# Kernel tuning notes

Measured on AMD Instinct MI355X. Metric: run time of the kernel, lower is better.

Reference implementation:

```python
import jax, jax.numpy as jnp
from jax import lax
import numpy as np

EPS = 1e-5

def _conv(x, w, b, s, p):
    # torch Conv2d: weight [O,I,kH,kW], NCHW
    y = lax.conv_general_dilated(x, w, (s, s), [(p, p), (p, p)],
                                 dimension_numbers=('NCHW', 'OIHW', 'NCHW'))
    return y + b[None, :, None, None]

def _convT(x, w, b, s, p):
    # torch ConvTranspose2d: weight [I,O,kH,kW]; equivalent to lhs-dilated conv
    wf = jnp.flip(w, (2, 3)).transpose(1, 0, 2, 3)  # -> [O,I,kH,kW]
    q = w.shape[2] - 1 - p
    y = lax.conv_general_dilated(x, wf, (1, 1), [(q, q), (q, q)],
                                 lhs_dilation=(s, s),
                                 dimension_numbers=('NCHW', 'OIHW', 'NCHW'))
    return y + b[None, :, None, None]

def _bn(x, g, b, m, v):
    # eval-mode BatchNorm2d with running stats
    s = g / jnp.sqrt(v + EPS)
    return x * s[None, :, None, None] + (b - m * s)[None, :, None, None]

def _forward(x, ew1, eb1, bn1g, bn1b, bn1m, bn1v, ew2, eb2, bn2g, bn2b, bn2m, bn2v,
             ew3, eb3, bn3g, bn3b, bn3m, bn3v, ew4, eb4, bn4g, bn4b, bn4m, bn4v,
             fc21w, fc21b, fc22w, fc22b, fc3w, fc3b,
             cw1, cb1, cbn1g, cbn1b, cbn1m, cbn1v, cw2, cb2, emb,
             dw1, db1, dbn1g, dbn1b, dbn1m, dbn1v, dw2, db2, dbn2g, dbn2b, dbn2m, dbn2v,
             dw3, db3, dbn3g, dbn3b, dbn3m, dbn3v, dw4, db4, dbn4g, dbn4b, dbn4m, dbn4v,
             ow, ob):
    relu = jax.nn.relu
    N = x.shape[0]
    # ---- encoder ----
    h = relu(_bn(_conv(x, ew1, eb1, 2, 1), bn1g, bn1b, bn1m, bn1v))   # [N,16,32,32]
    h = relu(_bn(_conv(h, ew2, eb2, 2, 1), bn2g, bn2b, bn2m, bn2v))   # [N,16,16,16]
    h = relu(_bn(_conv(h, ew3, eb3, 2, 1), bn3g, bn3b, bn3m, bn3v))   # [N,16,9,9]
    h = relu(_bn(_conv(h, ew4, eb4, 1, 0), bn4g, bn4b, bn4m, bn4v))   # [N,128,9,9]
    hl = h.reshape(N, -1)                                              # [N,10368]
    mu = hl @ fc21w + fc21b
    logvar = hl @ fc22w + fc22b
    z = mu  # eval-mode reparameterize returns mu
    # ---- vq_decode ----
    co = relu(z @ fc3w + fc3b)                                         # [N,10368]
    col = co.reshape(N, 128, 9, 9)
    ze = relu(_bn(_convT(col, cw1, cb1, 1, 0), cbn1g, cbn1b, cbn1m, cbn1v))
    z_e_x = _convT(ze, cw2, cb2, 1, 0)                                 # [N,32,9,9]
    zt = z_e_x.transpose(0, 2, 3, 1)                                   # [N,H,W,C]
    # ||z - e||^2 expanded (avoids [N,H,W,C,K] intermediate)
    d = ((zt * zt).sum(-1, keepdims=True)
         - 2.0 * jnp.einsum('nhwc,kc->nhwk', zt, emb)
         + (emb * emb).sum(-1))                                        # [N,H,W,K]
    latents = jnp.argmin(d, axis=-1)                                   # [N,H,W] int
    z_q = emb[latents]                                                 # [N,H,W,C]
    z_q_x = z_q.transpose(0, 3, 1, 2)                                  # [N,32,9,9]
    # ---- decoder ----
    g = relu(_bn(_convT(z_q_x, dw1, db1, 1, 0), dbn1g, dbn1b, dbn1m, dbn1v))  # [N,16,9,9]
    g = relu(_bn(_convT(g, dw2, db2, 2, 1), dbn2g, dbn2b, dbn2m, dbn2v))      # [N,16,18,18]
    g = relu(_bn(_convT(g, dw3, db3, 2, 1), dbn3g, dbn3b, dbn3m, dbn3v))      # [N,16,34,34]
    g = relu(_bn(_convT(g, dw4, db4, 2, 0), dbn4g, dbn4b, dbn4m, dbn4v))      # [N,16,68,68]
    x_tilde = _convT(g, ow, ob, 1, 0)                                         # [N,1,68,68]
    return (x_tilde, z, mu, logvar, z_e_x, z_q_x, latents)


def setup_inputs() -> dict:
    key = jax.random.key(0)
    ks = iter(jax.random.split(key, 64))
    def rn(shape, scale=0.05):
        return scale * jax.random.normal(next(ks), shape, jnp.float32)
    inp = {'x': jax.random.normal(next(ks), (512, 1, 64, 64), jnp.float32)}
    wspecs = {
        'ew1': (16, 1, 4, 4), 'eb1': (16,), 'ew2': (16, 16, 4, 4), 'eb2': (16,),
        'ew3': (16, 16, 2, 2), 'eb3': (16,), 'ew4': (128, 16, 1, 1), 'eb4': (128,),
        'fc21w': (10368, 64), 'fc21b': (64,), 'fc22w': (10368, 64), 'fc22b': (64,),
        'fc3w': (64, 10368), 'fc3b': (10368,),
        'cw1': (128, 32, 1, 1), 'cb1': (32,), 'cw2': (32, 32, 1, 1), 'cb2': (32,),
        'dw1': (32, 16, 1, 1), 'db1': (16,), 'dw2': (16, 16, 4, 4), 'db2': (16,),
        'dw3': (16, 16, 2, 2), 'db3': (16,), 'dw4': (16, 16, 2, 2), 'db4': (16,),
        'ow': (16, 1, 1, 1),
    }
    for n, s in wspecs.items():
        inp[n] = rn(s)
    inp['ob'] = jnp.full((1,), 0.5, jnp.float32)
    for ch, pre in [(16, 'bn1'), (16, 'bn2'), (16, 'bn3'), (128, 'bn4'), (32, 'cbn1'),
                    (16, 'dbn1'), (16, 'dbn2'), (16, 'dbn3'), (16, 'dbn4')]:
        inp[pre + 'g'] = jnp.ones((ch,), jnp.float32)
        inp[pre + 'b'] = jnp.zeros((ch,), jnp.float32)
        inp[pre + 'm'] = jnp.zeros((ch,), jnp.float32)
        inp[pre + 'v'] = jnp.ones((ch,), jnp.float32)
    inp['emb'] = rn((512, 32), 1.0 / 512)
    return inp


def reference(x, ew1, eb1, bn1g, bn1b, bn1m, bn1v, ew2, eb2, bn2g, bn2b, bn2m, bn2v,
              ew3, eb3, bn3g, bn3b, bn3m, bn3v, ew4, eb4, bn4g, bn4b, bn4m, bn4v,
              fc21w, fc21b, fc22w, fc22b, fc3w, fc3b,
              cw1, cb1, cbn1g, cbn1b, cbn1m, cbn1v, cw2, cb2, emb,
              dw1, db1, dbn1g, dbn1b, dbn1m, dbn1v, dw2, db2, dbn2g, dbn2b, dbn2m, dbn2v,
              dw3, db3, dbn3g, dbn3b, dbn3m, dbn3v, dw4, db4, dbn4g, dbn4b, dbn4m, dbn4v,
              ow, ob):
    return _forward(x, ew1, eb1, bn1g, bn1b, bn1m, bn1v, ew2, eb2, bn2g, bn2b, bn2m, bn2v,
                    ew3, eb3, bn3g, bn3b, bn3m, bn3v, ew4, eb4, bn4g, bn4b, bn4m, bn4v,
                    fc21w, fc21b, fc22w, fc22b, fc3w, fc3b,
                    cw1, cb1, cbn1g, cbn1b, cbn1m, cbn1v, cw2, cb2, emb,
                    dw1, db1, dbn1g, dbn1b, dbn1m, dbn1v, dw2, db2, dbn2g, dbn2b, dbn2m, dbn2v,
                    dw3, db3, dbn3g, dbn3b, dbn3m, dbn3v, dw4, db4, dbn4g, dbn4b, dbn4m, dbn4v,
                    ow, ob)
```

## Files before the change

kernel.cpp:

```cpp
#include <hip/hip_runtime.h>
#include <math.h>
#include <float.h>

#define BN_EPS 1e-5f

__device__ __forceinline__ float bn_apply(float y, float g, float b, float m, float v) {
  float s = g / sqrtf(v + BN_EPS);
  return y * s + (b - m * s);
}

__global__ void k_conv1(const float* __restrict__ x, const float* __restrict__ w,
                        const float* __restrict__ bias,
                        const float* __restrict__ g, const float* __restrict__ bb,
                        const float* __restrict__ bm, const float* __restrict__ bv,
                        float* __restrict__ out) {
  int t = blockIdx.x * 256 + threadIdx.x;
  int xo = t & 31, yo = (t >> 5) & 31, n = t >> 10;
  int iy0 = 2 * yo - 1, ix0 = 2 * xo - 1;
  const float* xb = x + n * 4096;
  float p[16];
#pragma unroll
  for (int ky = 0; ky < 4; ++ky)
#pragma unroll
    for (int kx = 0; kx < 4; ++kx) {
      int iy = iy0 + ky, ix = ix0 + kx;
      bool ok = (iy >= 0) & (iy < 64) & (ix >= 0) & (ix < 64);
      p[ky * 4 + kx] = ok ? xb[iy * 64 + ix] : 0.0f;
    }
  float* ob = out + n * 16384 + yo * 32 + xo;
#pragma unroll
  for (int o = 0; o < 16; ++o) {
    float acc = bias[o];
#pragma unroll
    for (int k = 0; k < 16; ++k) acc += p[k] * w[o * 16 + k];
    acc = bn_apply(acc, g[o], bb[o], bm[o], bv[o]);
    ob[o * 1024] = fmaxf(acc, 0.0f);
  }
}

__global__ void k_conv2(const float* __restrict__ A, const float* __restrict__ w,
                        const float* __restrict__ bias,
                        const float* __restrict__ g, const float* __restrict__ bb,
                        const float* __restrict__ bm, const float* __restrict__ bv,
                        float* __restrict__ out) {
  __shared__ float ws[4096];
  for (int i = threadIdx.x; i < 4096; i += 256) ws[i] = w[i];
  __syncthreads();
  int t = blockIdx.x * 256 + threadIdx.x;
  int x8 = t & 7, yo = (t >> 3) & 15, n = t >> 7;
  int iy0 = 2 * yo - 1;
  const float* Ab = A + n * 16384;
  float acc[2][16];
#pragma unroll
  for (int o = 0; o < 16; ++o) { float bvv = bias[o]; acc[0][o] = bvv; acc[1][o] = bvv; }
  for (int i = 0; i < 16; ++i) {
    float p[2][16];
#pragma unroll
    for (int px = 0; px < 2; ++px) {
      int ix0 = 2 * (x8 + px * 8) - 1;
#pragma unroll
      for (int ky = 0; ky < 4; ++ky)
#pragma unroll
        for (int kx = 0; kx < 4; ++kx) {
          int iy = iy0 + ky, ix = ix0 + kx;
          bool ok = (iy >= 0) & (iy < 32) & (ix >= 0) & (ix < 32);
          p[px][ky * 4 + kx] = ok ? Ab[i * 1024 + iy * 32 + ix] : 0.0f;
        }
    }
#pragma unroll
    for (int o = 0; o < 16; ++o) {
#pragma unroll
      for (int k = 0; k < 16; ++k) {
        float wv = ws[(o * 16 + i) * 16 + k];
        acc[0][o] += p[0][k] * wv;
        acc[1][o] += p[1][k] * wv;
      }
    }
  }
#pragma unroll
  for (int o = 0; o < 16; ++o) {
    float s = g[o] / sqrtf(bv[o] + BN_EPS);
    float sh = bb[o] - bm[o] * s;
    float* ob = out + (n * 16 + o) * 256 + yo * 16;
    ob[x8]     = fmaxf(acc[0][o] * s + sh, 0.0f);
    ob[x8 + 8] = fmaxf(acc[1][o] * s + sh, 0.0f);
  }
}

__global__ void __launch_bounds__(256) k_c34(const float* __restrict__ in,
    const float* __restrict__ w3, const float* __restrict__ b3,
    const float* __restrict__ g3, const float* __restrict__ bb3,
    const float* __restrict__ bm3, const float* __restrict__ bv3,
    const float* __restrict__ w4, const float* __restrict__ b4,
    const float* __restrict__ g4, const float* __restrict__ bb4,
    const float* __restrict__ bm4, const float* __restrict__ bv4,
    float* __restrict__ hl) {
  __shared__ float xin[4096];
  __shared__ float w3s[1024];
  __shared__ float c3s[16 * 81];
  __shared__ float k3a[16], k3b[16];
  __shared__ float k4a[128], k4b[128];
  int bx = blockIdx.x;
  int n = bx >> 1, half = bx & 1;
  int t = threadIdx.x;
  {
    const float4* iv = (const float4*)(in + n * 4096);
    float4* xv = (float4*)xin;
#pragma unroll
    for (int q = 0; q < 4; ++q) xv[t + 256 * q] = iv[t + 256 * q];
    if (t < 256) w3s[t] = w3[t];
    if (t >= 256 - 0) {}
    for (int i = t + 256; i < 1024; i += 256) w3s[i] = w3[i];
  }
  if (t < 16) {
    float s = g3[t] / sqrtf(bv3[t] + BN_EPS);
    k3a[t] = s;
    k3b[t] = b3[t] * s + (bb3[t] - bm3[t] * s);
  } else if (t >= 64 && t < 192) {
    int o = t - 64;
    float s = g4[o] / sqrtf(bv4[o] + BN_EPS);
    k4a[o] = s;
    k4b[o] = b4[o] * s + (bb4[o] - bm4[o] * s);
  }
  __syncthreads();
  for (int idx = t; idx < 1296; idx += 256) {
    int o = idx / 81, p = idx - o * 81;
    int yo = p / 9, xo = p - yo * 9;
    int iy0 = 2 * yo - 1, ix0 = 2 * xo - 1;
    bool ytop = iy0 >= 0, ybot = iy0 + 1 < 16;
    bool xlft = ix0 >= 0, xrgt = ix0 + 1 < 16;
    int iyt = ytop ? iy0 : 0, iyb = ybot ? iy0 + 1 : 15;
    int ixl = xlft ? ix0 : 0, ixr = xrgt ? ix0 + 1 : 15;
    float acc = 0.0f;
#pragma unroll
    for (int i = 0; i < 16; ++i) {
      const float* ch = xin + i * 256;
      float p0 = (ytop & xlft) ? ch[iyt * 16 + ixl] : 0.0f;
      float p1 = (ytop & xrgt) ? ch[iyt * 16 + ixr] : 0.0f;
      float p2 = (ybot & xlft) ? ch[iyb * 16 + ixl] : 0.0f;
      float p3 = (ybot & xrgt) ? ch[iyb * 16 + ixr] : 0.0f;
      float4 wv = *(const float4*)&w3s[(o * 16 + i) * 4];
      acc += p0 * wv.x + p1 * wv.y + p2 * wv.z + p3 * wv.w;
    }
    c3s[idx] = fmaxf(acc * k3a[o] + k3b[o], 0.0f);
  }
  __syncthreads();
  int lane = t & 63;
  int og = __builtin_amdgcn_readfirstlane(t >> 6);
  int o0 = half * 64 + og * 16;
  float* ob = hl + n * 10368;
#pragma unroll
  for (int pass = 0; pass < 2; ++pass) {
    int p = pass * 64 + lane;
    bool ok = p < 81; int pc = ok ? p : 80;
    float acc[16];
#pragma unroll
    for (int oo = 0; oo < 16; ++oo) acc[oo] = 0.0f;
#pragma unroll
    for (int i = 0; i < 16; ++i) {
      float v = c3s[i * 81 + pc];
#pragma unroll
      for (int oo = 0; oo < 16; ++oo)
        acc[oo] = fmaf(v, w4[(o0 + oo) * 16 + i], acc[oo]);
    }
    if (ok) {
#pragma unroll
      for (int oo = 0; oo < 16; ++oo) {
        int o = o0 + oo;
        ob[o * 81 + p] = fmaxf(acc[oo] * k4a[o] + k4b[o], 0.0f);
      }
    }
  }
}

__global__ void __launch_bounds__(256) k_gemm1(const float* __restrict__ hl,
                                               const float* __restrict__ w21,
                                               const float* __restrict__ w22,
                                               float* __restrict__ part) {
  __shared__ __align__(16) float hs[64 * 27];
  __shared__ __align__(16) float wsh[27 * 128];
  int kc = blockIdx.x, nt = blockIdx.y, t = threadIdx.x;
  int n0 = nt * 64, k0 = kc * 162;
  int jg = t & 31, ng = t >> 5;
  float acc[8][4];
#pragma unroll
  for (int i = 0; i < 8; ++i)
#pragma unroll
    for (int q = 0; q < 4; ++q) acc[i][q] = 0.0f;
  for (int s = 0; s < 6; ++s) {
    int ks = k0 + s * 27;
    __syncthreads();
    for (int idx = t; idx < 1728; idx += 256) {
      int r = idx / 27, c = idx - r * 27;
      hs[idx] = hl[(n0 + r) * 10368 + ks + c];
    }
    for (int idx = t; idx < 3456; idx += 256) {
      int r = idx >> 7, c = idx & 127;
      wsh[idx] = (c < 64) ? w21[(ks + r) * 64 + c] : w22[(ks + r) * 64 + (c - 64)];
    }
    __syncthreads();
#pragma unroll
    for (int kk = 0; kk < 27; ++kk) {
      float4 wv = *(const float4*)&wsh[kk * 128 + jg * 4];
#pragma unroll
      for (int i = 0; i < 8; ++i) {
        float h = hs[(ng * 8 + i) * 27 + kk];
        acc[i][0] = fmaf(h, wv.x, acc[i][0]);
        acc[i][1] = fmaf(h, wv.y, acc[i][1]);
        acc[i][2] = fmaf(h, wv.z, acc[i][2]);
        acc[i][3] = fmaf(h, wv.w, acc[i][3]);
      }
    }
  }
#pragma unroll
  for (int i = 0; i < 8; ++i) {
    int n = n0 + ng * 8 + i;
    float4 v = make_float4(acc[i][0], acc[i][1], acc[i][2], acc[i][3]);
    *(float4*)&part[(size_t)(kc * 512 + n) * 128 + jg * 4] = v;
  }
}

__global__ void k_fc_red(const float* __restrict__ part, const float* __restrict__ b21,
                         const float* __restrict__ b22, float* __restrict__ z,
                         float* __restrict__ mu, float* __restrict__ lv) {
  int t = blockIdx.x * 256 + threadIdx.x;
  int j = t & 127, n = t >> 7;
  float s = 0.0f;
  for (int kc = 0; kc < 64; ++kc) s += part[(size_t)(kc * 512 + n) * 128 + j];
  if (j < 64) { float r = s + b21[j]; z[n * 64 + j] = r; mu[n * 64 + j] = r; }
  else        { lv[n * 64 + (j - 64)] = s + b22[j - 64]; }
}

__global__ void k_fc3(const float* __restrict__ z, const float* __restrict__ w,
                      const float* __restrict__ b, float* __restrict__ E) {
  int m = blockIdx.x * 128 + threadIdx.x;
  int n0 = blockIdx.y * 32;
  float acc[32];
#pragma unroll
  for (int nn = 0; nn < 32; ++nn) acc[nn] = 0.0f;
  for (int j = 0; j < 64; ++j) {
    float wv = w[j * 10368 + m];
    const float* zb = z + n0 * 64 + j;
#pragma unroll
    for (int nn = 0; nn < 32; ++nn) acc[nn] += zb[nn * 64] * wv;
  }
  float bvv = b[m];
  float* Eb = E + n0 * 10368 + m;
#pragma unroll
  for (int nn = 0; nn < 32; ++nn) Eb[nn * 10368] = fmaxf(acc[nn] + bvv, 0.0f);
}

__global__ void __launch_bounds__(256) k_cw(const float* __restrict__ E,
                     const float* __restrict__ w1, const float* __restrict__ b1,
                     const float* __restrict__ g, const float* __restrict__ bb,
                     const float* __restrict__ bm, const float* __restrict__ bv,
                     const float* __restrict__ w2, const float* __restrict__ b2,
                     float* __restrict__ zex, float* __restrict__ zt) {
  __shared__ float ze_s[2592];
  int n = blockIdx.x, t = threadIdx.x;
  int lane = t & 63;
  int o0 = __builtin_amdgcn_readfirstlane(t >> 6) * 8;
  const float* co = E + n * 10368;
#pragma unroll
  for (int pass = 0; pass < 2; ++pass) {
    int p = pass * 64 + lane;
    bool ok = p < 81; int pc = ok ? p : 80;
    float acc[8];
#pragma unroll
    for (int oo = 0; oo < 8; ++oo) acc[oo] = b1[o0 + oo];
    for (int i = 0; i < 128; ++i) {
      float v = co[i * 81 + pc];
#pragma unroll
      for (int oo = 0; oo < 8; ++oo)
        acc[oo] = fmaf(v, w1[i * 32 + o0 + oo], acc[oo]);
    }
#pragma unroll
    for (int oo = 0; oo < 8; ++oo) {
      int o = o0 + oo;
      float r = bn_apply(acc[oo], g[o], bb[o], bm[o], bv[o]);
      if (ok) ze_s[o * 81 + p] = fmaxf(r, 0.0f);
    }
  }
  __syncthreads();
  float* zb = zex + n * 2592;
  float* ztb = zt + n * 81 * 32;
#pragma unroll
  for (int pass = 0; pass < 2; ++pass) {
    int p = pass * 64 + lane;
    bool ok = p < 81; int pc = ok ? p : 80;
    float acc[8];
#pragma unroll
    for (int oo = 0; oo < 8; ++oo) acc[oo] = b2[o0 + oo];
    for (int j = 0; j < 32; ++j) {
      float v = ze_s[j * 81 + pc];
#pragma unroll
      for (int oo = 0; oo < 8; ++oo)
        acc[oo] = fmaf(v, w2[j * 32 + o0 + oo], acc[oo]);
    }
    if (ok) {
#pragma unroll
      for (int oo = 0; oo < 8; ++oo) {
        zb[(o0 + oo) * 81 + p] = acc[oo];
        ztb[p * 32 + o0 + oo] = acc[oo];
      }
    }
  }
}

__global__ void k_ee(const float* __restrict__ emb, float* __restrict__ ee) {
  int k = blockIdx.x * 256 + threadIdx.x;
  if (k < 512) {
    const float4* e = (const float4*)(emb + k * 32);
    float s = 0.0f;
#pragma unroll
    for (int q = 0; q < 8; ++q) {
      float4 v = e[q];
      s += v.x * v.x + v.y * v.y + v.z * v.z + v.w * v.w;
    }
    ee[k] = s;
  }
}

__global__ void __launch_bounds__(256) k_vq2(const float* __restrict__ zt,
                                             const float* __restrict__ emb,
                                             const float* __restrict__ ee,
                                             float* __restrict__ lat_out,
                                             float* __restrict__ zqx) {
  __shared__ float bd_s[4][64];
  __shared__ int   bi_s[4][64];
  __shared__ int   bif[64];
  int t = threadIdx.x;
  int lane = t & 63, sub = t >> 6;
  int sub_u = __builtin_amdgcn_readfirstlane(sub);
  int pix = blockIdx.x * 64 + lane;
  float z[32];
  {
    const float4* zr = (const float4*)(zt + (size_t)pix * 32);
#pragma unroll
    for (int q = 0; q < 8; ++q) {
      float4 v = zr[q];
      z[q * 4] = v.x; z[q * 4 + 1] = v.y; z[q * 4 + 2] = v.z; z[q * 4 + 3] = v.w;
    }
  }
  const float* ebase = emb + sub_u * 128 * 32;
  const float* eeb   = ee + sub_u * 128;
  int kbase = sub_u * 128;
  float best = FLT_MAX;
  int bi = kbase;
  for (int kk = 0; kk < 128; kk += 2) {
    const float* e0 = ebase + kk * 32;
    const float* e1 = e0 + 32;
    float d0a = 0.f, d0b = 0.f, d1a = 0.f, d1b = 0.f;
#pragma unroll
    for (int c = 0; c < 32; c += 2) {
      d0a = fmaf(z[c], e0[c], d0a);
      d0b = fmaf(z[c + 1], e0[c + 1], d0b);
      d1a = fmaf(z[c], e1[c], d1a);
      d1b = fmaf(z[c + 1], e1[c + 1], d1b);
    }
    float d0 = fmaf(-2.0f, d0a + d0b, eeb[kk]);
    float d1 = fmaf(-2.0f, d1a + d1b, eeb[kk + 1]);
    if (d0 < best) { best = d0; bi = kbase + kk; }
    if (d1 < best) { best = d1; bi = kbase + kk + 1; }
  }
  bd_s[sub][lane] = best;
  bi_s[sub][lane] = bi;
  __syncthreads();
  if (t < 64) {
    float bd = bd_s[0][t]; int b = bi_s[0][t];
#pragma unroll
    for (int q = 1; q < 4; ++q)
      if (bd_s[q][t] < bd) { bd = bd_s[q][t]; b = bi_s[q][t]; }
    lat_out[blockIdx.x * 64 + t] = (float)b;
    bif[t] = b;
  }
  __syncthreads();
  int pix0 = blockIdx.x * 64;
  for (int idx = t; idx < 2048; idx += 256) {
    int c = idx >> 6, pl = idx & 63;
    int pg = pix0 + pl;
    int n = pg / 81, p = pg - n * 81;
    zqx[n * 2592 + c * 81 + p] = emb[bif[pl] * 32 + c];
  }
}

__global__ void k_dw1(const float* __restrict__ in, const float* __restrict__ w,
                      const float* __restrict__ bias,
                      const float* __restrict__ g, const float* __restrict__ bb,
                      const float* __restrict__ bm, const float* __restrict__ bv,
                      float* __restrict__ out) {
  __shared__ float ws[512];
  for (int i = threadIdx.x; i < 512; i += 256) ws[i] = w[i];
  __syncthreads();
  int t = blockIdx.x * 256 + threadIdx.x;
  int p = t % 81; int o = (t / 81) & 15; int n = t / 1296;
  const float* ib = in + n * 2592 + p;
  float acc = bias[o];
#pragma unroll
  for (int i = 0; i < 32; ++i) acc += ib[i * 81] * ws[i * 16 + o];
  float r = bn_apply(acc, g[o], bb[o], bm[o], bv[o]);
  out[t] = fmaxf(r, 0.0f);
}

__global__ void __launch_bounds__(256) k_dw2(const float* __restrict__ in,
                      const float* __restrict__ w, const float* __restrict__ bias,
                      const float* __restrict__ g, const float* __restrict__ bb,
                      const float* __restrict__ bm, const float* __restrict__ bv,
                      float* __restrict__ out) {
  int t = threadIdx.x;
  int lane = t & 63;
  int og = __builtin_amdgcn_readfirstlane(t >> 6);
  int idx = blockIdx.x * 64 + lane;
  int n = idx / 81, blk = idx - n * 81;
  int iy = blk / 9, ix = blk - iy * 9;
  const float* ib = in + n * 1296;
  int r0 = iy - 1, r2 = iy + 1, c0 = ix - 1, c2 = ix + 1;
  bool r0ok = r0 >= 0, r2ok = r2 < 9, c0ok = c0 >= 0, c2ok = c2 < 9;
  int r0c = r0ok ? r0 : 0, r2c = r2ok ? r2 : 8;
  int c0c = c0ok ? c0 : 0, c2c = c2ok ? c2 : 8;
  float acc[4][2][2];
#pragma unroll
  for (int oo = 0; oo < 4; ++oo)
#pragma unroll
    for (int dy = 0; dy < 2; ++dy)
#pragma unroll
      for (int dx = 0; dx < 2; ++dx) acc[oo][dy][dx] = 0.0f;
  for (int i = 0; i < 16; ++i) {
    const float* ch = ib + i * 81;
    float v[3][3];
    v[1][1] = ch[iy * 9 + ix];
    v[1][0] = c0ok ? ch[iy * 9 + c0c] : 0.0f;
    v[1][2] = c2ok ? ch[iy * 9 + c2c] : 0.0f;
    v[0][1] = r0ok ? ch[r0c * 9 + ix] : 0.0f;
    v[0][0] = (r0ok & c0ok) ? ch[r0c * 9 + c0c] : 0.0f;
    v[0][2] = (r0ok & c2ok) ? ch[r0c * 9 + c2c] : 0.0f;
    v[2][1] = r2ok ? ch[r2c * 9 + ix] : 0.0f;
    v[2][0] = (r2ok & c0ok) ? ch[r2c * 9 + c0c] : 0.0f;
    v[2][2] = (r2ok & c2ok) ? ch[r2c * 9 + c2c] : 0.0f;
    const float* wb = w + (i * 16 + og * 4) * 16;
#pragma unroll
    for (int oo = 0; oo < 4; ++oo) {
      const float* wo = wb + oo * 16;
      acc[oo][0][0] = fmaf(v[1][1], wo[1 * 4 + 1], acc[oo][0][0]);
      acc[oo][0][0] = fmaf(v[1][0], wo[1 * 4 + 3], acc[oo][0][0]);
      acc[oo][0][0] = fmaf(v[0][1], wo[3 * 4 + 1], acc[oo][0][0]);
      acc[oo][0][0] = fmaf(v[0][0], wo[3 * 4 + 3], acc[oo][0][0]);
      acc[oo][0][1] = fmaf(v[1][1], wo[1 * 4 + 2], acc[oo][0][1]);
      acc[oo][0][1] = fmaf(v[1][2], wo[1 * 4 + 0], acc[oo][0][1]);
      acc[oo][0][1] = fmaf(v[0][1], wo[3 * 4 + 2], acc[oo][0][1]);
      acc[oo][0][1] = fmaf(v[0][2], wo[3 * 4 + 0], acc[oo][0][1]);
      acc[oo][1][0] = fmaf(v[1][1], wo[2 * 4 + 1], acc[oo][1][0]);
      acc[oo][1][0] = fmaf(v[1][0], wo[2 * 4 + 3], acc[oo][1][0]);
      acc[oo][1][0] = fmaf(v[2][1], wo[0 * 4 + 1], acc[oo][1][0]);
      acc[oo][1][0] = fmaf(v[2][0], wo[0 * 4 + 3], acc[oo][1][0]);
      acc[oo][1][1] = fmaf(v[1][1], wo[2 * 4 + 2], acc[oo][1][1]);
      acc[oo][1][1] = fmaf(v[1][2], wo[2 * 4 + 0], acc[oo][1][1]);
      acc[oo][1][1] = fmaf(v[2][1], wo[0 * 4 + 2], acc[oo][1][1]);
      acc[oo][1][1] = fmaf(v[2][2], wo[0 * 4 + 0], acc[oo][1][1]);
    }
  }
  float* ob = out + n * 5184 + (2 * iy) * 18 + 2 * ix;
#pragma unroll
  for (int oo = 0; oo < 4; ++oo) {
    int o = og * 4 + oo;
    float s = g[o] / sqrtf(bv[o] + BN_EPS);
    float sh = bb[o] - bm[o] * s;
    float bo = bias[o];
    float r00 = fmaxf((acc[oo][0][0] + bo) * s + sh, 0.0f);
    float r01 = fmaxf((acc[oo][0][1] + bo) * s + sh, 0.0f);
    float r10 = fmaxf((acc[oo][1][0] + bo) * s + sh, 0.0f);
    float r11 = fmaxf((acc[oo][1][1] + bo) * s + sh, 0.0f);
    float* op = ob + o * 324;
    *(float2*)&op[0]  = make_float2(r00, r01);
    *(float2*)&op[18] = make_float2(r10, r11);
  }
}

__global__ void k_dw3(const float* __restrict__ in, const float* __restrict__ w,
                      const float* __restrict__ bias,
                      const float* __restrict__ g, const float* __restrict__ bb,
                      const float* __restrict__ bm, const float* __restrict__ bv,
                      float* __restrict__ out) {
  int t = blockIdx.x * 256 + threadIdx.x;
  int ii = t % 324; int n = t / 324;
  int iy = ii / 18, ix = ii % 18;
  const float* ib = in + n * 5184 + iy * 18 + ix;
  float acc[4][16];
#pragma unroll
  for (int a = 0; a < 4; ++a)
#pragma unroll
    for (int o = 0; o < 16; ++o) acc[a][o] = 0.0f;
  for (int i = 0; i < 16; ++i) {
    float v = ib[i * 324];
    const float4* wr = (const float4*)(w + i * 64);
#pragma unroll
    for (int o = 0; o < 16; ++o) {
      float4 wt = wr[o];
      acc[0][o] = fmaf(v, wt.x, acc[0][o]);
      acc[1][o] = fmaf(v, wt.y, acc[1][o]);
      acc[2][o] = fmaf(v, wt.z, acc[2][o]);
      acc[3][o] = fmaf(v, wt.w, acc[3][o]);
    }
  }
  int yo0 = 2 * iy - 1, xo0 = 2 * ix - 1;
  float* ob = out + n * 18496;
#pragma unroll
  for (int o = 0; o < 16; ++o) {
    float s = g[o] / sqrtf(bv[o] + BN_EPS);
    float sh = bb[o] - bm[o] * s;
    float bo = bias[o];
#pragma unroll
    for (int a = 0; a < 2; ++a)
#pragma unroll
      for (int b = 0; b < 2; ++b) {
        int yo = yo0 + a, xo = xo0 + b;
        if (yo >= 0 && yo < 34 && xo >= 0 && xo < 34)
          ob[o * 1156 + yo * 34 + xo] = fmaxf((acc[a * 2 + b][o] + bo) * s + sh, 0.0f);
      }
  }
}

__global__ void k_dw4ow(const float* __restrict__ in, const float* __restrict__ w,
                        const float* __restrict__ bias,
                        const float* __restrict__ g, const float* __restrict__ bb,
                        const float* __restrict__ bm, const float* __restrict__ bv,
                        const float* __restrict__ oww, const float* __restrict__ obb,
                        float* __restrict__ out) {
  int t = blockIdx.x * 256 + threadIdx.x;
  int ii = t % 1156; int n = t / 1156;
  int iy = ii / 34, ix = ii % 34;
  const float* ib = in + n * 18496 + iy * 34 + ix;
  float acc[4][16];
#pragma unroll
  for (int a = 0; a < 4; ++a)
#pragma unroll
    for (int o = 0; o < 16; ++o) acc[a][o] = 0.0f;
  for (int i = 0; i < 16; ++i) {
    float v = ib[i * 1156];
    const float4* wr = (const float4*)(w + i * 64);
#pragma unroll
    for (int o = 0; o < 16; ++o) {
      float4 wt = wr[o];
      acc[0][o] = fmaf(v, wt.x, acc[0][o]);
      acc[1][o] = fmaf(v, wt.y, acc[1][o]);
      acc[2][o] = fmaf(v, wt.z, acc[2][o]);
      acc[3][o] = fmaf(v, wt.w, acc[3][o]);
    }
  }
  float r[4];
#pragma unroll
  for (int a = 0; a < 4; ++a) r[a] = obb[0];
#pragma unroll
  for (int o = 0; o < 16; ++o) {
    float s = g[o] / sqrtf(bv[o] + BN_EPS);
    float sh = bb[o] - bm[o] * s;
    float bo = bias[o];
    float wo = oww[o];
#pragma unroll
    for (int a = 0; a < 4; ++a)
      r[a] += fmaxf((acc[a][o] + bo) * s + sh, 0.0f) * wo;
  }
  float* ob = out + n * 4624 + 2 * ix;
  *(float2*)&ob[(2 * iy) * 68]     = make_float2(r[0], r[1]);
  *(float2*)&ob[(2 * iy + 1) * 68] = make_float2(r[2], r[3]);
}

extern "C" void kernel_launch(void* const* d_in, const int* in_sizes, int n_in,
                              void* d_out, int out_size, void* d_ws, size_t ws_size,
                              hipStream_t stream) {
  const float* x     = (const float*)d_in[0];
  const float* ew1   = (const float*)d_in[1];
  const float* eb1   = (const float*)d_in[2];
  const float* ew2   = (const float*)d_in[3];
  const float* eb2   = (const float*)d_in[4];
  const float* ew3   = (const float*)d_in[5];
  const float* eb3   = (const float*)d_in[6];
  const float* ew4   = (const float*)d_in[7];
  const float* eb4   = (const float*)d_in[8];
  const float* fc21w = (const float*)d_in[9];
  const float* fc21b = (const float*)d_in[10];
  const float* fc22w = (const float*)d_in[11];
  const float* fc22b = (const float*)d_in[12];
  const float* fc3w  = (const float*)d_in[13];
  const float* fc3b  = (const float*)d_in[14];
  const float* cw1   = (const float*)d_in[15];
  const float* cb1   = (const float*)d_in[16];
  const float* cw2   = (const float*)d_in[17];
  const float* cb2   = (const float*)d_in[18];
  const float* dw1   = (const float*)d_in[19];
  const float* db1   = (const float*)d_in[20];
  const float* dw2   = (const float*)d_in[21];
  const float* db2   = (const float*)d_in[22];
  const float* dw3   = (const float*)d_in[23];
  const float* db3   = (const float*)d_in[24];
  const float* dw4   = (const float*)d_in[25];
  const float* db4   = (const float*)d_in[26];
  const float* oww   = (const float*)d_in[27];
  const float* obb   = (const float*)d_in[28];
  const float* bn1g  = (const float*)d_in[29];
  const float* bn1b  = (const float*)d_in[30];
  const float* bn1m  = (const float*)d_in[31];
  const float* bn1v  = (const float*)d_in[32];
  const float* bn2g  = (const float*)d_in[33];
  const float* bn2b  = (const float*)d_in[34];
  const float* bn2m  = (const float*)d_in[35];
  const float* bn2v  = (const float*)d_in[36];
  const float* bn3g  = (const float*)d_in[37];
  const float* bn3b  = (const float*)d_in[38];
  const float* bn3m  = (const float*)d_in[39];
  const float* bn3v  = (const float*)d_in[40];
  const float* bn4g  = (const float*)d_in[41];
  const float* bn4b  = (const float*)d_in[42];
  const float* bn4m  = (const float*)d_in[43];
  const float* bn4v  = (const float*)d_in[44];
  const float* cbn1g = (const float*)d_in[45];
  const float* cbn1b = (const float*)d_in[46];
  const float* cbn1m = (const float*)d_in[47];
  const float* cbn1v = (const float*)d_in[48];
  const float* dbn1g = (const float*)d_in[49];
  const float* dbn1b = (const float*)d_in[50];
  const float* dbn1m = (const float*)d_in[51];
  const float* dbn1v = (const float*)d_in[52];
  const float* dbn2g = (const float*)d_in[53];
  const float* dbn2b = (const float*)d_in[54];
  const float* dbn2m = (const float*)d_in[55];
  const float* dbn2v = (const float*)d_in[56];
  const float* dbn3g = (const float*)d_in[57];
  const float* dbn3b = (const float*)d_in[58];
  const float* dbn3m = (const float*)d_in[59];
  const float* dbn3v = (const float*)d_in[60];
  const float* dbn4g = (const float*)d_in[61];
  const float* dbn4b = (const float*)d_in[62];
  const float* dbn4m = (const float*)d_in[63];
  const float* dbn4v = (const float*)d_in[64];
  const float* emb   = (const float*)d_in[65];

  float* out = (float*)d_out;
  float* xt_o  = out;
  float* z_o   = out + 2367488;
  float* mu_o  = out + 2400256;
  float* lv_o  = out + 2433024;
  float* zex_o = out + 2465792;
  float* zqx_o = out + 3792896;
  float* lat_o = out + 5120000;

  float* ws = (float*)d_ws;
  float* A    = ws;
  float* Bt   = ws + 8388608;
  float* Dhl  = ws + 663552;
  float* part = ws + 5971968;
  float* Eco  = ws;
  float* zt   = ws + 10166272;
  float* eev  = ws + 11493376;
  float* G    = ws + 5308416;
  float* H    = ws + 5971968;
  float* I    = ws + 8626176;

  k_conv1<<<2048, 256, 0, stream>>>(x, ew1, eb1, bn1g, bn1b, bn1m, bn1v, A);
  k_conv2<<<256, 256, 0, stream>>>(A, ew2, eb2, bn2g, bn2b, bn2m, bn2v, Bt);
  k_c34<<<1024, 256, 0, stream>>>(Bt, ew3, eb3, bn3g, bn3b, bn3m, bn3v,
                                  ew4, eb4, bn4g, bn4b, bn4m, bn4v, Dhl);
  k_gemm1<<<dim3(64, 8), 256, 0, stream>>>(Dhl, fc21w, fc22w, part);
  k_fc_red<<<256, 256, 0, stream>>>(part, fc21b, fc22b, z_o, mu_o, lv_o);
  k_ee<<<2, 256, 0, stream>>>(emb, eev);
  k_fc3<<<dim3(81, 16), 128, 0, stream>>>(z_o, fc3w, fc3b, Eco);
  k_cw<<<512, 256, 0, stream>>>(Eco, cw1, cb1, cbn1g, cbn1b, cbn1m, cbn1v, cw2, cb2, zex_o, zt);
  k_vq2<<<648, 256, 0, stream>>>(zt, emb, eev, lat_o, zqx_o);
  k_dw1<<<2592, 256, 0, stream>>>(zqx_o, dw1, db1, dbn1g, dbn1b, dbn1m, dbn1v, G);
  k_dw2<<<648, 256, 0, stream>>>(G, dw2, db2, dbn2g, dbn2b, dbn2m, dbn2v, H);
  k_dw3<<<648, 256, 0, stream>>>(H, dw3, db3, dbn3g, dbn3b, dbn3m, dbn3v, I);
  k_dw4ow<<<2312, 256, 0, stream>>>(I, dw4, db4, dbn4g, dbn4b, dbn4m, dbn4v, oww, obb, xt_o);
}
```

Baseline: 504.3 us.

## Register-prefetch next k-slice in fc GEMM and transpose activation tile in LDS

The fc21/fc22 GEMM kernel now loads the next 27-wide k-slice of activations and weights into registers while the current slice is being computed. This software pipeline is meant to hide global-memory latency. The activation tile is stored transposed in shared memory with a padded stride of 68, so each thread reads its 8 rows with two float4 loads instead of 8 scalar loads. The extra prefetch registers add register pressure and may lower occupancy. A redundant weight-copy loop in the encoder kernel is also simplified.

```diff
diff --git a/kernel.cpp b/kernel.cpp
--- a/kernel.cpp
+++ b/kernel.cpp
@@ -108,9 +108,7 @@
     float4* xv = (float4*)xin;
 #pragma unroll
     for (int q = 0; q < 4; ++q) xv[t + 256 * q] = iv[t + 256 * q];
-    if (t < 256) w3s[t] = w3[t];
-    if (t >= 256 - 0) {}
-    for (int i = t + 256; i < 1024; i += 256) w3s[i] = w3[i];
+    for (int i = t; i < 1024; i += 256) w3s[i] = w3[i];
   }
   if (t < 16) {
     float s = g3[t] / sqrtf(bv3[t] + BN_EPS);
@@ -177,7 +175,7 @@
                                                const float* __restrict__ w21,
                                                const float* __restrict__ w22,
                                                float* __restrict__ part) {
-  __shared__ __align__(16) float hs[64 * 27];
+  __shared__ __align__(16) float hs[27 * 68];
   __shared__ __align__(16) float wsh[27 * 128];
   int kc = blockIdx.x, nt = blockIdx.y, t = threadIdx.x;
   int n0 = nt * 64, k0 = kc * 162;
@@ -187,36 +185,70 @@
   for (int i = 0; i < 8; ++i)
 #pragma unroll
     for (int q = 0; q < 4; ++q) acc[i][q] = 0.0f;
+  float ph[7], pw[14];
+  {
+    int ks = k0;
+#pragma unroll
+    for (int q = 0; q < 7; ++q) {
+      int idx = t + q * 256;
+      if (idx < 1728) { int nr = idx / 27, kk = idx - nr * 27;
+        ph[q] = hl[(n0 + nr) * 10368 + ks + kk]; }
+    }
+#pragma unroll
+    for (int q = 0; q < 14; ++q) {
+      int idx = t + q * 256;
+      if (idx < 3456) { int r = idx >> 7, c = idx & 127;
+        pw[q] = (c < 64) ? w21[(ks + r) * 64 + c] : w22[(ks + r) * 64 + (c - 64)]; }
+    }
+  }
   for (int s = 0; s < 6; ++s) {
-    int ks = k0 + s * 27;
     __syncthreads();
-    for (int idx = t; idx < 1728; idx += 256) {
-      int r = idx / 27, c = idx - r * 27;
-      hs[idx] = hl[(n0 + r) * 10368 + ks + c];
-    }
-    for (int idx = t; idx < 3456; idx += 256) {
-      int r = idx >> 7, c = idx & 127;
-      wsh[idx] = (c < 64) ? w21[(ks + r) * 64 + c] : w22[(ks + r) * 64 + (c - 64)];
+#pragma unroll
+    for (int q = 0; q < 7; ++q) {
+      int idx = t + q * 256;
+      if (idx < 1728) { int nr = idx / 27, kk = idx - nr * 27; hs[kk * 68 + nr] = ph[q]; }
+    }
+#pragma unroll
+    for (int q = 0; q < 14; ++q) {
+      int idx = t + q * 256;
+      if (idx < 3456) wsh[idx] = pw[q];
     }
     __syncthreads();
-#pragma unroll
+    if (s < 5) {
+      int ks = k0 + (s + 1) * 27;
+#pragma unroll
+      for (int q = 0; q < 7; ++q) {
+        int idx = t + q * 256;
+        if (idx < 1728) { int nr = idx / 27, kk = idx - nr * 27;
+          ph[q] = hl[(n0 + nr) * 10368 + ks + kk]; }
+      }
+#pragma unroll
+      for (int q = 0; q < 14; ++q) {
+        int idx = t + q * 256;
+        if (idx < 3456) { int r = idx >> 7, c = idx & 127;
+          pw[q] = (c < 64) ? w21[(ks + r) * 64 + c] : w22[(ks + r) * 64 + (c - 64)]; }
+      }
+    }
+#pragma unroll 9
     for (int kk = 0; kk < 27; ++kk) {
+      float4 h0 = *(const float4*)&hs[kk * 68 + ng * 8];
+      float4 h1 = *(const float4*)&hs[kk * 68 + ng * 8 + 4];
       float4 wv = *(const float4*)&wsh[kk * 128 + jg * 4];
+      float hv[8] = {h0.x, h0.y, h0.z, h0.w, h1.x, h1.y, h1.z, h1.w};
 #pragma unroll
       for (int i = 0; i < 8; ++i) {
-        float h = hs[(ng * 8 + i) * 27 + kk];
-        acc[i][0] = fmaf(h, wv.x, acc[i][0]);
-        acc[i][1] = fmaf(h, wv.y, acc[i][1]);
-        acc[i][2] = fmaf(h, wv.z, acc[i][2]);
-        acc[i][3] = fmaf(h, wv.w, acc[i][3]);
+        acc[i][0] = fmaf(hv[i], wv.x, acc[i][0]);
+        acc[i][1] = fmaf(hv[i], wv.y, acc[i][1]);
+        acc[i][2] = fmaf(hv[i], wv.z, acc[i][2]);
+        acc[i][3] = fmaf(hv[i], wv.w, acc[i][3]);
       }
     }
   }
 #pragma unroll
   for (int i = 0; i < 8; ++i) {
     int n = n0 + ng * 8 + i;
-    float4 v = make_float4(acc[i][0], acc[i][1], acc[i][2], acc[i][3]);
-    *(float4*)&part[(size_t)(kc * 512 + n) * 128 + jg * 4] = v;
+    *(float4*)&part[(size_t)(kc * 512 + n) * 128 + jg * 4] =
+        make_float4(acc[i][0], acc[i][1], acc[i][2], acc[i][3]);
   }
 }
 
```

New measurement: 486.9 us. -3.5%, faster.
